# Performance work log

Measured on AMD Instinct MI355X. Metric: run time of the kernel, lower is better.

Reference implementation:

```python
import jax, jax.numpy as jnp
import numpy as np

D = 128
N = 262144

def setup_inputs() -> dict:
    key = jax.random.key(0)
    ks = jax.random.split(key, 10)
    inp = {
        'member_embeddings': 0.1 * jax.random.normal(ks[0], (N, D), dtype=jnp.float32),
        'item_embedding': 0.1 * jax.random.normal(ks[1], (D,), dtype=jnp.float32),
        # nn.Linear params (torch convention: y = x @ W.T + b)
        'W_c1': jax.random.normal(ks[2], (D, D), dtype=jnp.float32) / np.sqrt(D),
        'b_c1': jnp.zeros((D,), dtype=jnp.float32),
        'W_c2': jax.random.normal(ks[3], (D, D), dtype=jnp.float32) / np.sqrt(D),
        'b_c2': jnp.zeros((D,), dtype=jnp.float32),
        'w_pa': jax.random.normal(ks[4], (D,), dtype=jnp.float32) / np.sqrt(D),  # peer_attention weight (1,D) squeezed
        'b_pa': jnp.zeros((), dtype=jnp.float32),
        'w_vc': jax.random.normal(ks[5], (D,), dtype=jnp.float32) / np.sqrt(D),  # v_c weight (1,D) squeezed
        'b_vc': jnp.zeros((), dtype=jnp.float32),
    }
    return inp

def reference(member_embeddings, item_embedding, W_c1, b_c1, W_c2, b_c2, w_pa, b_pa, w_vc, b_vc):
    E = member_embeddings  # [N, D]
    # SP: self persistence scores  alpha_SP_i = u_i^T v
    sp = E @ item_embedding  # [N]
    # Peer scores are per-member scalars shared across all exclusion sets.
    s = E @ w_pa + b_pa                       # [N]
    m = jnp.max(s)
    e = jnp.exp(s - m)                        # [N]
    S = jnp.sum(e)                            # scalar
    eE = e[:, None] * E                       # [N, D]
    sum_eE = jnp.sum(eE, axis=0)              # [D]
    # softmax over peers excluding i (exact: softmax is shift-invariant)
    denom = S - e                             # [N]
    peer_agg = (sum_eE[None, :] - eE) / denom[:, None]  # [N, D]
    # PI: v_c^T ReLU(W_c1 u_i + W_c2 peer_agg_i + b)
    h = E @ W_c1.T + b_c1 + peer_agg @ W_c2.T + b_c2     # [N, D]
    pi = jax.nn.relu(h) @ w_vc + b_vc                    # [N]  (dropout = identity in eval)
    alpha = jnp.float32(1.0)
    beta = jnp.float32(1.0)
    attention_weights = jax.nn.softmax(alpha * sp + beta * pi, axis=0)  # [N]
    group_embedding = attention_weights @ E               # [D]
    return (group_embedding, attention_weights)
```

## Files before the change

### kernel.cpp

```cpp
#include <hip/hip_runtime.h>

#define DIM 128

typedef __attribute__((ext_vector_type(8))) short bf16x8;
typedef __attribute__((ext_vector_type(4))) float f32x4;

#define WS_B12    0
#define WS_C      128
#define WS_SUMEE  256
#define WS_S      384
#define WS_ZB     416
#define WS_GEB    512
#define WS_WBF    4608
#define WS_EEP    20992
#define WS_SEP    152064
#define WS_SP     153088
#define WS_E      415232
#define WS_WEXP   677376

__device__ __forceinline__ unsigned short f2bf(float f) {
    union { float f; unsigned u; } v; v.f = f;
    unsigned r = v.u + 0x7fffu + ((v.u >> 16) & 1u);
    return (unsigned short)(r >> 16);
}

__device__ __forceinline__ float bfbits(unsigned u) {
    union { unsigned u; float f; } v; v.u = u;
    return v.f;
}

__global__ __launch_bounds__(256) void k1_init(const float* __restrict__ Wc1,
                                               const float* __restrict__ Wc2,
                                               const float* __restrict__ bc1,
                                               const float* __restrict__ bc2,
                                               float* __restrict__ ws) {
    int gid = blockIdx.x * 256 + threadIdx.x;
    unsigned short* wbf = (unsigned short*)(ws + WS_WBF);
    if (gid < 32768) {
        int n = gid >> 7, k = gid & 127;
        float v = (n < 128) ? Wc1[n * 128 + k] : Wc2[(n - 128) * 128 + k];
        wbf[gid] = f2bf(v);
    }
    if (gid < 4096) ws[WS_GEB + gid] = 0.f;
    if (gid < 128) ws[WS_B12 + gid] = bc1[gid] + bc2[gid];
    if (gid < 64) ws[WS_ZB + gid] = 0.f;
}

__global__ __launch_bounds__(256) void k2_stats(const float* __restrict__ E,
                                                const float* __restrict__ v,
                                                const float* __restrict__ wpa,
                                                const float* __restrict__ bpa,
                                                float* __restrict__ ws) {
    __shared__ float red[16][128];
    __shared__ float redS[16];
    int t = threadIdx.x;
    int wave = t >> 6, lane = t & 63;
    int cl = lane & 15, rs = lane >> 4;
    int row0 = blockIdx.x * 256;
    const float4* E4 = (const float4*)E;

    float4 va = ((const float4*)v)[cl];
    float4 vb = ((const float4*)v)[16 + cl];
    float4 pa = ((const float4*)wpa)[cl];
    float4 pb = ((const float4*)wpa)[16 + cl];
    float bias = bpa[0];

    float4 acc0 = {0.f, 0.f, 0.f, 0.f}, acc1 = {0.f, 0.f, 0.f, 0.f};
    float se = 0.f;
    float* sp_ws = ws + WS_SP;
    float* e_ws = ws + WS_E;

#pragma unroll 4
    for (int it = 0; it < 16; ++it) {
        int row = row0 + it * 16 + wave * 4 + rs;
        float4 x0 = E4[row * 32 + cl];
        float4 x1 = E4[row * 32 + 16 + cl];
        float dv = x0.x * va.x + x0.y * va.y + x0.z * va.z + x0.w * va.w
                 + x1.x * vb.x + x1.y * vb.y + x1.z * vb.z + x1.w * vb.w;
        float dp = x0.x * pa.x + x0.y * pa.y + x0.z * pa.z + x0.w * pa.w
                 + x1.x * pb.x + x1.y * pb.y + x1.z * pb.z + x1.w * pb.w;
        for (int off = 1; off < 16; off <<= 1) {
            dv += __shfl_xor(dv, off);
            dp += __shfl_xor(dp, off);
        }
        float e = __expf(dp + bias);
        if (cl == 0) {
            sp_ws[row] = dv;
            e_ws[row] = e;
            se += e;
        }
        acc0.x += e * x0.x; acc0.y += e * x0.y; acc0.z += e * x0.z; acc0.w += e * x0.w;
        acc1.x += e * x1.x; acc1.y += e * x1.y; acc1.z += e * x1.z; acc1.w += e * x1.w;
    }
    int rr = wave * 4 + rs;
    float* dst = red[rr];
    dst[cl * 4 + 0] = acc0.x; dst[cl * 4 + 1] = acc0.y;
    dst[cl * 4 + 2] = acc0.z; dst[cl * 4 + 3] = acc0.w;
    dst[64 + cl * 4 + 0] = acc1.x; dst[64 + cl * 4 + 1] = acc1.y;
    dst[64 + cl * 4 + 2] = acc1.z; dst[64 + cl * 4 + 3] = acc1.w;
    if (cl == 0) redS[rr] = se;
    __syncthreads();
    if (t < 128) {
        float s = 0.f;
#pragma unroll
        for (int r = 0; r < 16; ++r) s += red[r][t];
        ws[WS_EEP + t * 1024 + blockIdx.x] = s;
    }
    if (t == 0) {
        float s = 0.f;
#pragma unroll
        for (int r = 0; r < 16; ++r) s += redS[r];
        ws[WS_SEP + blockIdx.x] = s;
    }
}

__global__ __launch_bounds__(256) void k2b_reduce(float* __restrict__ ws) {
    __shared__ float r4[4];
    int t = threadIdx.x, blk = blockIdx.x;
    const float* src = (blk < 128) ? (ws + WS_EEP + blk * 1024) : (ws + WS_SEP);
    float s = src[t] + src[t + 256] + src[t + 512] + src[t + 768];
    for (int off = 1; off < 64; off <<= 1) s += __shfl_xor(s, off);
    if ((t & 63) == 0) r4[t >> 6] = s;
    __syncthreads();
    if (t == 0) {
        float tot = r4[0] + r4[1] + r4[2] + r4[3];
        if (blk < 128) ws[WS_SUMEE + blk] = tot;
        else ws[WS_S] = tot;
    }
}

__global__ __launch_bounds__(128) void k3_c(const float* __restrict__ Wc2,
                                            float* __restrict__ ws) {
    int j = threadIdx.x;
    const float4* row = (const float4*)(Wc2 + j * 128);
    const float4* se = (const float4*)(ws + WS_SUMEE);
    float4 s4 = {0.f, 0.f, 0.f, 0.f};
#pragma unroll
    for (int k = 0; k < 32; ++k) {
        float4 a = row[k], b = se[k];
        s4.x += a.x * b.x; s4.y += a.y * b.y; s4.z += a.z * b.z; s4.w += a.w * b.w;
    }
    ws[WS_C + j] = s4.x + s4.y + s4.z + s4.w;
}

__global__ __launch_bounds__(512, 6) void k4_main(const float* __restrict__ E,
                                                  const float* __restrict__ wvc,
                                                  const float* __restrict__ bvc_p,
                                                  float* __restrict__ ws) {
    __shared__ unsigned short Elds[64 * 136];
    __shared__ float pim[8][64];
    __shared__ float gep[8][128];
    __shared__ float e_lds[64], dinv_lds[64];
    __shared__ float zw[8];

    int t = threadIdx.x;
    int w = t >> 6, lane = t & 63, cl = lane & 15, q = lane >> 4;
    int row0 = blockIdx.x * 64;
    const unsigned short* wbf = (const unsigned short*)(ws + WS_WBF);

    int j = w * 16 + cl;
    float cj = ws[WS_C + j];
    float b12j = ws[WS_B12 + j];
    float wvcj = wvc[j];
    float bvc = bvc_p[0];
    int r0 = w * 8 + q * 2;
    float sp0 = ws[WS_SP + row0 + r0];
    float sp1 = ws[WS_SP + row0 + r0 + 1];

    bf16x8 bfr[2][4];
#pragma unroll
    for (int c2 = 0; c2 < 2; ++c2) {
        int ct = w + c2 * 8;
#pragma unroll
        for (int kt = 0; kt < 4; ++kt)
            bfr[c2][kt] = *(const bf16x8*)(wbf + (ct * 16 + cl) * 128 + kt * 32 + q * 8);
    }

    const float4* E4 = (const float4*)E + (size_t)row0 * 32;
#pragma unroll
    for (int i = 0; i < 4; ++i) {
        int idx = t + 512 * i;
        int row = idx >> 5, kq = idx & 31;
        float4 x = E4[idx];
        unsigned p0 = (unsigned)f2bf(x.x) | ((unsigned)f2bf(x.y) << 16);
        unsigned p1 = (unsigned)f2bf(x.z) | ((unsigned)f2bf(x.w) << 16);
        *(uint2*)&Elds[row * 136 + kq * 4] = make_uint2(p0, p1);
    }
    if (t < 64) {
        float Sv = ws[WS_S];
        float ev = ws[WS_E + row0 + t];
        e_lds[t] = ev;
        dinv_lds[t] = 1.0f / (Sv - ev);
    }
    __syncthreads();

    f32x4 acc[4][2];
#pragma unroll
    for (int rt = 0; rt < 4; ++rt) {
        acc[rt][0] = (f32x4){0.f, 0.f, 0.f, 0.f};
        acc[rt][1] = (f32x4){0.f, 0.f, 0.f, 0.f};
    }
#pragma unroll
    for (int rt = 0; rt < 4; ++rt) {
        bf16x8 a[4];
#pragma unroll
        for (int kt = 0; kt < 4; ++kt)
            a[kt] = *(const bf16x8*)&Elds[(rt * 16 + cl) * 136 + kt * 32 + q * 8];
#pragma unroll
        for (int kt = 0; kt < 4; ++kt) {
            acc[rt][0] = __builtin_amdgcn_mfma_f32_16x16x32_bf16(a[kt], bfr[0][kt], acc[rt][0], 0, 0, 0);
            acc[rt][1] = __builtin_amdgcn_mfma_f32_16x16x32_bf16(a[kt], bfr[1][kt], acc[rt][1], 0, 0, 0);
        }
    }

#pragma unroll
    for (int rt = 0; rt < 4; ++rt) {
#pragma unroll
        for (int reg = 0; reg < 4; ++reg) {
            int row_it = rt * 16 + q * 4 + reg;
            float er = e_lds[row_it];
            float dinv = dinv_lds[row_it];
            float h = acc[rt][0][reg] + b12j + (cj - er * acc[rt][1][reg]) * dinv;
            float p = wvcj * fmaxf(h, 0.f);
            p += __shfl_xor(p, 1);
            p += __shfl_xor(p, 2);
            p += __shfl_xor(p, 4);
            p += __shfl_xor(p, 8);
            if (cl == 0) pim[w][row_it] = p;
        }
    }
    __syncthreads();

    float pi0 = 0.f, pi1 = 0.f;
#pragma unroll
    for (int wv = 0; wv < 8; ++wv) {
        pi0 += pim[wv][r0];
        pi1 += pim[wv][r0 + 1];
    }
    float we0 = __expf(sp0 + bvc + pi0);
    float we1 = __expf(sp1 + bvc + pi1);
    if (cl == 0) {
        ws[WS_WEXP + row0 + r0] = we0;
        ws[WS_WEXP + row0 + r0 + 1] = we1;
    }
    float z = we0 + we1;
    z += __shfl_xor(z, 16);
    z += __shfl_xor(z, 32);
    if (lane == 0) zw[w] = z;

    float acc8[8] = {0.f, 0.f, 0.f, 0.f, 0.f, 0.f, 0.f, 0.f};
#pragma unroll
    for (int rr = 0; rr < 2; ++rr) {
        int r = r0 + rr;
        float wer = rr ? we1 : we0;
        uint4 u = *(const uint4*)&Elds[r * 136 + cl * 8];
        acc8[0] += wer * bfbits(u.x << 16);
        acc8[1] += wer * bfbits(u.x & 0xffff0000u);
        acc8[2] += wer * bfbits(u.y << 16);
        acc8[3] += wer * bfbits(u.y & 0xffff0000u);
        acc8[4] += wer * bfbits(u.z << 16);
        acc8[5] += wer * bfbits(u.z & 0xffff0000u);
        acc8[6] += wer * bfbits(u.w << 16);
        acc8[7] += wer * bfbits(u.w & 0xffff0000u);
    }
#pragma unroll
    for (int jj = 0; jj < 8; ++jj) {
        acc8[jj] += __shfl_xor(acc8[jj], 16);
        acc8[jj] += __shfl_xor(acc8[jj], 32);
    }
    if (lane < 16) {
        *(float4*)&gep[w][cl * 8] = (float4){acc8[0], acc8[1], acc8[2], acc8[3]};
        *(float4*)&gep[w][cl * 8 + 4] = (float4){acc8[4], acc8[5], acc8[6], acc8[7]};
    }
    __syncthreads();

    if (t < 128) {
        float tot = 0.f;
#pragma unroll
        for (int wv = 0; wv < 8; ++wv) tot += gep[wv][t];
        atomicAdd(&ws[WS_GEB + (blockIdx.x & 31) * 128 + t], tot);
    }
    if (t == 128) {
        float zs = zw[0] + zw[1] + zw[2] + zw[3] + zw[4] + zw[5] + zw[6] + zw[7];
        atomicAdd(&ws[WS_ZB + (blockIdx.x & 63)], zs);
    }
}

__global__ __launch_bounds__(256) void k5_final(const float* __restrict__ ws,
                                                float* __restrict__ out) {
    int t = threadIdx.x, blk = blockIdx.x;
    float z = ws[WS_ZB + (t & 63)];
    for (int off = 1; off < 64; off <<= 1) z += __shfl_xor(z, off);
    float invZ = 1.0f / z;
    if (blk < 1024) {
        int i = blk * 256 + t;
        out[128 + i] = ws[WS_WEXP + i] * invZ;
    } else if (t < 128) {
        float s = 0.f;
#pragma unroll
        for (int b = 0; b < 32; ++b) s += ws[WS_GEB + b * 128 + t];
        out[t] = s * invZ;
    }
}

extern "C" void kernel_launch(void* const* d_in, const int* in_sizes, int n_in,
                              void* d_out, int out_size, void* d_ws, size_t ws_size,
                              hipStream_t stream) {
    const float* E   = (const float*)d_in[0];
    const float* v   = (const float*)d_in[1];
    const float* Wc1 = (const float*)d_in[2];
    const float* bc1 = (const float*)d_in[3];
    const float* Wc2 = (const float*)d_in[4];
    const float* bc2 = (const float*)d_in[5];
    const float* wpa = (const float*)d_in[6];
    const float* bpa = (const float*)d_in[7];
    const float* wvc = (const float*)d_in[8];
    const float* bvc = (const float*)d_in[9];
    float* ws  = (float*)d_ws;
    float* out = (float*)d_out;

    k1_init<<<128, 256, 0, stream>>>(Wc1, Wc2, bc1, bc2, ws);
    k2_stats<<<1024, 256, 0, stream>>>(E, v, wpa, bpa, ws);
    k2b_reduce<<<129, 256, 0, stream>>>(ws);
    k3_c<<<1, 128, 0, stream>>>(Wc2, ws);
    k4_main<<<4096, 512, 0, stream>>>(E, wvc, bvc, ws);
    k5_final<<<1025, 256, 0, stream>>>(ws, out);
}
```

Measured before the change: 274.8 us.

## Write bf16 copy of E in stats pass and read it directly in main kernel

The stats kernel now also writes a bf16 copy of the member embeddings to workspace, and the main kernel reads MFMA A-operands and the weighted-sum rows from that copy in global memory instead of re-reading fp32 E and staging it through LDS. This halves the main kernel's read traffic and removes its LDS staging and one barrier. In exchange it adds a 64 MB write in the stats pass, and its operand loads become uncoalesced, strided global loads that are likely to be served from L2. The launch-bounds occupancy hint drops from 6 to 4, and the workspace must be large enough for the new buffer.

```diff
diff --git a/kernel.cpp b/kernel.cpp
--- a/kernel.cpp
+++ b/kernel.cpp
@@ -17,6 +17,7 @@
 #define WS_SP     153088
 #define WS_E      415232
 #define WS_WEXP   677376
+#define WS_EBF    939520
 
 __device__ __forceinline__ unsigned short f2bf(float f) {
     union { float f; unsigned u; } v; v.f = f;
@@ -58,6 +59,7 @@
     int cl = lane & 15, rs = lane >> 4;
     int row0 = blockIdx.x * 256;
     const float4* E4 = (const float4*)E;
+    unsigned short* ebf = (unsigned short*)(ws + WS_EBF);
 
     float4 va = ((const float4*)v)[cl];
     float4 vb = ((const float4*)v)[16 + cl];
@@ -75,6 +77,14 @@
         int row = row0 + it * 16 + wave * 4 + rs;
         float4 x0 = E4[row * 32 + cl];
         float4 x1 = E4[row * 32 + 16 + cl];
+        unsigned p0 = (unsigned)f2bf(x0.x) | ((unsigned)f2bf(x0.y) << 16);
+        unsigned p1 = (unsigned)f2bf(x0.z) | ((unsigned)f2bf(x0.w) << 16);
+        unsigned p2 = (unsigned)f2bf(x1.x) | ((unsigned)f2bf(x1.y) << 16);
+        unsigned p3 = (unsigned)f2bf(x1.z) | ((unsigned)f2bf(x1.w) << 16);
+        unsigned short* er = ebf + (size_t)row * 128;
+        *(uint2*)(er + cl * 4) = make_uint2(p0, p1);
+        *(uint2*)(er + 64 + cl * 4) = make_uint2(p2, p3);
+
         float dv = x0.x * va.x + x0.y * va.y + x0.z * va.z + x0.w * va.w
                  + x1.x * vb.x + x1.y * vb.y + x1.z * vb.z + x1.w * vb.w;
         float dp = x0.x * pa.x + x0.y * pa.y + x0.z * pa.z + x0.w * pa.w
@@ -143,11 +153,9 @@
     ws[WS_C + j] = s4.x + s4.y + s4.z + s4.w;
 }
 
-__global__ __launch_bounds__(512, 6) void k4_main(const float* __restrict__ E,
-                                                  const float* __restrict__ wvc,
+__global__ __launch_bounds__(512, 4) void k4_main(const float* __restrict__ wvc,
                                                   const float* __restrict__ bvc_p,
                                                   float* __restrict__ ws) {
-    __shared__ unsigned short Elds[64 * 136];
     __shared__ float pim[8][64];
     __shared__ float gep[8][128];
     __shared__ float e_lds[64], dinv_lds[64];
@@ -157,6 +165,7 @@
     int w = t >> 6, lane = t & 63, cl = lane & 15, q = lane >> 4;
     int row0 = blockIdx.x * 64;
     const unsigned short* wbf = (const unsigned short*)(ws + WS_WBF);
+    const unsigned short* ebf = (const unsigned short*)(ws + WS_EBF);
 
     int j = w * 16 + cl;
     float cj = ws[WS_C + j];
@@ -176,23 +185,12 @@
             bfr[c2][kt] = *(const bf16x8*)(wbf + (ct * 16 + cl) * 128 + kt * 32 + q * 8);
     }
 
-    const float4* E4 = (const float4*)E + (size_t)row0 * 32;
-#pragma unroll
-    for (int i = 0; i < 4; ++i) {
-        int idx = t + 512 * i;
-        int row = idx >> 5, kq = idx & 31;
-        float4 x = E4[idx];
-        unsigned p0 = (unsigned)f2bf(x.x) | ((unsigned)f2bf(x.y) << 16);
-        unsigned p1 = (unsigned)f2bf(x.z) | ((unsigned)f2bf(x.w) << 16);
-        *(uint2*)&Elds[row * 136 + kq * 4] = make_uint2(p0, p1);
-    }
     if (t < 64) {
         float Sv = ws[WS_S];
         float ev = ws[WS_E + row0 + t];
         e_lds[t] = ev;
         dinv_lds[t] = 1.0f / (Sv - ev);
     }
-    __syncthreads();
 
     f32x4 acc[4][2];
 #pragma unroll
@@ -202,16 +200,18 @@
     }
 #pragma unroll
     for (int rt = 0; rt < 4; ++rt) {
+        const unsigned short* arow = ebf + (size_t)(row0 + rt * 16 + cl) * 128 + q * 8;
         bf16x8 a[4];
 #pragma unroll
         for (int kt = 0; kt < 4; ++kt)
-            a[kt] = *(const bf16x8*)&Elds[(rt * 16 + cl) * 136 + kt * 32 + q * 8];
+            a[kt] = *(const bf16x8*)(arow + kt * 32);
 #pragma unroll
         for (int kt = 0; kt < 4; ++kt) {
             acc[rt][0] = __builtin_amdgcn_mfma_f32_16x16x32_bf16(a[kt], bfr[0][kt], acc[rt][0], 0, 0, 0);
             acc[rt][1] = __builtin_amdgcn_mfma_f32_16x16x32_bf16(a[kt], bfr[1][kt], acc[rt][1], 0, 0, 0);
         }
     }
+    __syncthreads();
 
 #pragma unroll
     for (int rt = 0; rt < 4; ++rt) {
@@ -251,9 +251,8 @@
     float acc8[8] = {0.f, 0.f, 0.f, 0.f, 0.f, 0.f, 0.f, 0.f};
 #pragma unroll
     for (int rr = 0; rr < 2; ++rr) {
-        int r = r0 + rr;
         float wer = rr ? we1 : we0;
-        uint4 u = *(const uint4*)&Elds[r * 136 + cl * 8];
+        uint4 u = *(const uint4*)(ebf + (size_t)(row0 + r0 + rr) * 128 + cl * 8);
         acc8[0] += wer * bfbits(u.x << 16);
         acc8[1] += wer * bfbits(u.x & 0xffff0000u);
         acc8[2] += wer * bfbits(u.y << 16);
@@ -323,6 +322,6 @@
     k2_stats<<<1024, 256, 0, stream>>>(E, v, wpa, bpa, ws);
     k2b_reduce<<<129, 256, 0, stream>>>(ws);
     k3_c<<<1, 128, 0, stream>>>(Wc2, ws);
-    k4_main<<<4096, 512, 0, stream>>>(E, wvc, bvc, ws);
+    k4_main<<<4096, 512, 0, stream>>>(wvc, bvc, ws);
     k5_final<<<1025, 256, 0, stream>>>(ws, out);
 }
```

After: 327.2 us. 1.19x slower.

## Restructure main kernel into smaller blocks with swizzled LDS and tree reduction

Applied to the files above, without the earlier changes.

The main kernel now runs 256-thread blocks over 32 rows each. Each wave keeps its A fragments in registers and loops over two column groups, loading the W fragments per pass instead of holding all B fragments resident. The LDS tile drops its padding and uses an XOR swizzle to avoid bank conflicts. The group-embedding atomics are replaced by per-block partial writes plus a separate reduction kernel, and the stats kernel uses twice as many blocks. These changes aim to raise occupancy and remove atomic contention, at the cost of an extra launch, more workspace traffic and repeated weight loads from cache.

```diff
diff --git a/kernel.cpp b/kernel.cpp
--- a/kernel.cpp
+++ b/kernel.cpp
@@ -1,27 +1,26 @@
 #include <hip/hip_runtime.h>
-
-#define DIM 128
 
 typedef __attribute__((ext_vector_type(8))) short bf16x8;
 typedef __attribute__((ext_vector_type(4))) float f32x4;
 
 #define WS_B12    0
-#define WS_C      128
-#define WS_SUMEE  256
-#define WS_S      384
-#define WS_ZB     416
-#define WS_GEB    512
-#define WS_WBF    4608
-#define WS_EEP    20992
-#define WS_SEP    152064
-#define WS_SP     153088
-#define WS_E      415232
-#define WS_WEXP   677376
-
-__device__ __forceinline__ unsigned short f2bf(float f) {
+#define WS_CPK    128
+#define WS_SUMEE  640
+#define WS_S      768
+#define WS_ZB     800
+#define WS_WBF    896
+#define WS_EEP    17280
+#define WS_SEP    279424
+#define WS_SP     281472
+#define WS_E      543616
+#define WS_WEXP   805760
+#define WS_GOUT   1067904
+#define WS_G2     2116480
+
+__device__ __forceinline__ unsigned f2bf(float f) {
     union { float f; unsigned u; } v; v.f = f;
     unsigned r = v.u + 0x7fffu + ((v.u >> 16) & 1u);
-    return (unsigned short)(r >> 16);
+    return r >> 16;
 }
 
 __device__ __forceinline__ float bfbits(unsigned u) {
@@ -39,9 +38,8 @@
     if (gid < 32768) {
         int n = gid >> 7, k = gid & 127;
         float v = (n < 128) ? Wc1[n * 128 + k] : Wc2[(n - 128) * 128 + k];
-        wbf[gid] = f2bf(v);
-    }
-    if (gid < 4096) ws[WS_GEB + gid] = 0.f;
+        wbf[gid] = (unsigned short)f2bf(v);
+    }
     if (gid < 128) ws[WS_B12 + gid] = bc1[gid] + bc2[gid];
     if (gid < 64) ws[WS_ZB + gid] = 0.f;
 }
@@ -56,7 +54,7 @@
     int t = threadIdx.x;
     int wave = t >> 6, lane = t & 63;
     int cl = lane & 15, rs = lane >> 4;
-    int row0 = blockIdx.x * 256;
+    int row0 = blockIdx.x * 128;
     const float4* E4 = (const float4*)E;
 
     float4 va = ((const float4*)v)[cl];
@@ -71,7 +69,7 @@
     float* e_ws = ws + WS_E;
 
 #pragma unroll 4
-    for (int it = 0; it < 16; ++it) {
+    for (int it = 0; it < 8; ++it) {
         int row = row0 + it * 16 + wave * 4 + rs;
         float4 x0 = E4[row * 32 + cl];
         float4 x1 = E4[row * 32 + 16 + cl];
@@ -104,7 +102,7 @@
         float s = 0.f;
 #pragma unroll
         for (int r = 0; r < 16; ++r) s += red[r][t];
-        ws[WS_EEP + t * 1024 + blockIdx.x] = s;
+        ws[WS_EEP + t * 2048 + blockIdx.x] = s;
     }
     if (t == 0) {
         float s = 0.f;
@@ -117,8 +115,10 @@
 __global__ __launch_bounds__(256) void k2b_reduce(float* __restrict__ ws) {
     __shared__ float r4[4];
     int t = threadIdx.x, blk = blockIdx.x;
-    const float* src = (blk < 128) ? (ws + WS_EEP + blk * 1024) : (ws + WS_SEP);
-    float s = src[t] + src[t + 256] + src[t + 512] + src[t + 768];
+    const float* src = (blk < 128) ? (ws + WS_EEP + blk * 2048) : (ws + WS_SEP);
+    float s = 0.f;
+#pragma unroll
+    for (int k = 0; k < 8; ++k) s += src[t + 256 * k];
     for (int off = 1; off < 64; off <<= 1) s += __shfl_xor(s, off);
     if ((t & 63) == 0) r4[t >> 6] = s;
     __syncthreads();
@@ -130,6 +130,7 @@
 }
 
 __global__ __launch_bounds__(128) void k3_c(const float* __restrict__ Wc2,
+                                            const float* __restrict__ wvc,
                                             float* __restrict__ ws) {
     int j = threadIdx.x;
     const float4* row = (const float4*)(Wc2 + j * 128);
@@ -140,109 +141,107 @@
         float4 a = row[k], b = se[k];
         s4.x += a.x * b.x; s4.y += a.y * b.y; s4.z += a.z * b.z; s4.w += a.w * b.w;
     }
-    ws[WS_C + j] = s4.x + s4.y + s4.z + s4.w;
-}
-
-__global__ __launch_bounds__(512, 6) void k4_main(const float* __restrict__ E,
-                                                  const float* __restrict__ wvc,
+    float cj = s4.x + s4.y + s4.z + s4.w;
+    *(float4*)(ws + WS_CPK + j * 4) = (float4){cj, ws[WS_B12 + j], wvc[j], 0.f};
+}
+
+__global__ __launch_bounds__(256, 4) void k4_main(const float* __restrict__ E,
                                                   const float* __restrict__ bvc_p,
                                                   float* __restrict__ ws) {
-    __shared__ unsigned short Elds[64 * 136];
-    __shared__ float pim[8][64];
-    __shared__ float gep[8][128];
-    __shared__ float e_lds[64], dinv_lds[64];
-    __shared__ float zw[8];
+    __shared__ unsigned short Elds[32 * 128];
+    __shared__ float pim[4][32];
+    __shared__ float gep[4][128];
+    __shared__ float zw[4];
 
     int t = threadIdx.x;
     int w = t >> 6, lane = t & 63, cl = lane & 15, q = lane >> 4;
-    int row0 = blockIdx.x * 64;
+    int row0 = blockIdx.x * 32;
     const unsigned short* wbf = (const unsigned short*)(ws + WS_WBF);
 
-    int j = w * 16 + cl;
-    float cj = ws[WS_C + j];
-    float b12j = ws[WS_B12 + j];
-    float wvcj = wvc[j];
+    const float4* E4 = (const float4*)E + (size_t)row0 * 32;
+#pragma unroll
+    for (int i = 0; i < 4; ++i) {
+        int idx = t + 256 * i;
+        int row = idx >> 5, kq = idx & 31;
+        float4 x = E4[idx];
+        unsigned p0 = f2bf(x.x) | (f2bf(x.y) << 16);
+        unsigned p1 = f2bf(x.z) | (f2bf(x.w) << 16);
+        int cc = (kq >> 1) ^ ((row & 1) << 2);
+        *(uint2*)&Elds[row * 128 + cc * 8 + (kq & 1) * 4] = make_uint2(p0, p1);
+    }
+
+    float Sv = ws[WS_S];
     float bvc = bvc_p[0];
+    float4 eA = *(const float4*)(ws + WS_E + row0 + q * 4);
+    float4 eB = *(const float4*)(ws + WS_E + row0 + 16 + q * 4);
+    float dinvA[4], dinvB[4];
+#pragma unroll
+    for (int r = 0; r < 4; ++r) {
+        dinvA[r] = 1.0f / (Sv - ((const float*)&eA)[r]);
+        dinvB[r] = 1.0f / (Sv - ((const float*)&eB)[r]);
+    }
     int r0 = w * 8 + q * 2;
     float sp0 = ws[WS_SP + row0 + r0];
     float sp1 = ws[WS_SP + row0 + r0 + 1];
-
-    bf16x8 bfr[2][4];
-#pragma unroll
-    for (int c2 = 0; c2 < 2; ++c2) {
-        int ct = w + c2 * 8;
+    __syncthreads();
+
+    bf16x8 a[2][4];
+#pragma unroll
+    for (int rt = 0; rt < 2; ++rt) {
+        int row = rt * 16 + cl;
+        int sw = (row & 1) << 2;
+        const unsigned short* rbase = Elds + row * 128;
 #pragma unroll
         for (int kt = 0; kt < 4; ++kt)
-            bfr[c2][kt] = *(const bf16x8*)(wbf + (ct * 16 + cl) * 128 + kt * 32 + q * 8);
-    }
-
-    const float4* E4 = (const float4*)E + (size_t)row0 * 32;
-#pragma unroll
-    for (int i = 0; i < 4; ++i) {
-        int idx = t + 512 * i;
-        int row = idx >> 5, kq = idx & 31;
-        float4 x = E4[idx];
-        unsigned p0 = (unsigned)f2bf(x.x) | ((unsigned)f2bf(x.y) << 16);
-        unsigned p1 = (unsigned)f2bf(x.z) | ((unsigned)f2bf(x.w) << 16);
-        *(uint2*)&Elds[row * 136 + kq * 4] = make_uint2(p0, p1);
-    }
-    if (t < 64) {
-        float Sv = ws[WS_S];
-        float ev = ws[WS_E + row0 + t];
-        e_lds[t] = ev;
-        dinv_lds[t] = 1.0f / (Sv - ev);
-    }
-    __syncthreads();
-
-    f32x4 acc[4][2];
-#pragma unroll
-    for (int rt = 0; rt < 4; ++rt) {
-        acc[rt][0] = (f32x4){0.f, 0.f, 0.f, 0.f};
-        acc[rt][1] = (f32x4){0.f, 0.f, 0.f, 0.f};
-    }
-#pragma unroll
-    for (int rt = 0; rt < 4; ++rt) {
-        bf16x8 a[4];
-#pragma unroll
-        for (int kt = 0; kt < 4; ++kt)
-            a[kt] = *(const bf16x8*)&Elds[(rt * 16 + cl) * 136 + kt * 32 + q * 8];
+            a[rt][kt] = *(const bf16x8*)(rbase + ((((kt << 2) + q) ^ sw) << 3));
+    }
+
+    float pirow[2][4] = {{0.f, 0.f, 0.f, 0.f}, {0.f, 0.f, 0.f, 0.f}};
+#pragma unroll 1
+    for (int pp = 0; pp < 2; ++pp) {
+        int j = (w + pp * 4) * 16 + cl;
+        float4 cc = *(const float4*)(ws + WS_CPK + j * 4);
+        bf16x8 b0[4], b1[4];
 #pragma unroll
         for (int kt = 0; kt < 4; ++kt) {
-            acc[rt][0] = __builtin_amdgcn_mfma_f32_16x16x32_bf16(a[kt], bfr[0][kt], acc[rt][0], 0, 0, 0);
-            acc[rt][1] = __builtin_amdgcn_mfma_f32_16x16x32_bf16(a[kt], bfr[1][kt], acc[rt][1], 0, 0, 0);
-        }
-    }
-
-#pragma unroll
-    for (int rt = 0; rt < 4; ++rt) {
+            b0[kt] = *(const bf16x8*)(wbf + (size_t)j * 128 + kt * 32 + q * 8);
+            b1[kt] = *(const bf16x8*)(wbf + (size_t)(128 + j) * 128 + kt * 32 + q * 8);
+        }
+#pragma unroll
+        for (int rt = 0; rt < 2; ++rt) {
+            f32x4 acc0 = {0.f, 0.f, 0.f, 0.f}, acc1 = {0.f, 0.f, 0.f, 0.f};
+#pragma unroll
+            for (int kt = 0; kt < 4; ++kt) {
+                acc0 = __builtin_amdgcn_mfma_f32_16x16x32_bf16(a[rt][kt], b0[kt], acc0, 0, 0, 0);
+                acc1 = __builtin_amdgcn_mfma_f32_16x16x32_bf16(a[rt][kt], b1[kt], acc1, 0, 0, 0);
+            }
+            const float* ee = rt ? (const float*)&eB : (const float*)&eA;
+            const float* dd = rt ? dinvB : dinvA;
+#pragma unroll
+            for (int reg = 0; reg < 4; ++reg) {
+                float h = acc0[reg] + cc.y + (cc.x - ee[reg] * acc1[reg]) * dd[reg];
+                pirow[rt][reg] += cc.z * fmaxf(h, 0.f);
+            }
+        }
+    }
+#pragma unroll
+    for (int rt = 0; rt < 2; ++rt)
 #pragma unroll
         for (int reg = 0; reg < 4; ++reg) {
-            int row_it = rt * 16 + q * 4 + reg;
-            float er = e_lds[row_it];
-            float dinv = dinv_lds[row_it];
-            float h = acc[rt][0][reg] + b12j + (cj - er * acc[rt][1][reg]) * dinv;
-            float p = wvcj * fmaxf(h, 0.f);
+            float p = pirow[rt][reg];
             p += __shfl_xor(p, 1);
             p += __shfl_xor(p, 2);
             p += __shfl_xor(p, 4);
             p += __shfl_xor(p, 8);
-            if (cl == 0) pim[w][row_it] = p;
-        }
-    }
-    __syncthreads();
-
-    float pi0 = 0.f, pi1 = 0.f;
-#pragma unroll
-    for (int wv = 0; wv < 8; ++wv) {
-        pi0 += pim[wv][r0];
-        pi1 += pim[wv][r0 + 1];
-    }
+            if (cl == 0) pim[w][rt * 16 + q * 4 + reg] = p;
+        }
+    __syncthreads();
+
+    float pi0 = pim[0][r0] + pim[1][r0] + pim[2][r0] + pim[3][r0];
+    float pi1 = pim[0][r0 + 1] + pim[1][r0 + 1] + pim[2][r0 + 1] + pim[3][r0 + 1];
     float we0 = __expf(sp0 + bvc + pi0);
     float we1 = __expf(sp1 + bvc + pi1);
-    if (cl == 0) {
-        ws[WS_WEXP + row0 + r0] = we0;
-        ws[WS_WEXP + row0 + r0 + 1] = we1;
-    }
+    if (cl == 0) *(float2*)(ws + WS_WEXP + row0 + r0) = make_float2(we0, we1);
     float z = we0 + we1;
     z += __shfl_xor(z, 16);
     z += __shfl_xor(z, 32);
@@ -253,7 +252,8 @@
     for (int rr = 0; rr < 2; ++rr) {
         int r = r0 + rr;
         float wer = rr ? we1 : we0;
-        uint4 u = *(const uint4*)&Elds[r * 136 + cl * 8];
+        int cc = cl ^ (rr << 2);
+        uint4 u = *(const uint4*)(Elds + r * 128 + cc * 8);
         acc8[0] += wer * bfbits(u.x << 16);
         acc8[1] += wer * bfbits(u.x & 0xffff0000u);
         acc8[2] += wer * bfbits(u.y << 16);
@@ -275,15 +275,20 @@
     __syncthreads();
 
     if (t < 128) {
-        float tot = 0.f;
-#pragma unroll
-        for (int wv = 0; wv < 8; ++wv) tot += gep[wv][t];
-        atomicAdd(&ws[WS_GEB + (blockIdx.x & 31) * 128 + t], tot);
-    }
-    if (t == 128) {
-        float zs = zw[0] + zw[1] + zw[2] + zw[3] + zw[4] + zw[5] + zw[6] + zw[7];
-        atomicAdd(&ws[WS_ZB + (blockIdx.x & 63)], zs);
-    }
+        float tot = gep[0][t] + gep[1][t] + gep[2][t] + gep[3][t];
+        ws[WS_GOUT + (size_t)blockIdx.x * 128 + t] = tot;
+    }
+    if (t == 0)
+        atomicAdd(&ws[WS_ZB + (blockIdx.x & 63)], zw[0] + zw[1] + zw[2] + zw[3]);
+}
+
+__global__ __launch_bounds__(128) void k4b_ge(float* __restrict__ ws) {
+    int t = threadIdx.x, b = blockIdx.x;
+    const float* src = ws + WS_GOUT + (size_t)b * 32 * 128;
+    float s = 0.f;
+#pragma unroll 8
+    for (int k = 0; k < 32; ++k) s += src[k * 128 + t];
+    ws[WS_G2 + b * 128 + t] = s;
 }
 
 __global__ __launch_bounds__(256) void k5_final(const float* __restrict__ ws,
@@ -297,8 +302,8 @@
         out[128 + i] = ws[WS_WEXP + i] * invZ;
     } else if (t < 128) {
         float s = 0.f;
-#pragma unroll
-        for (int b = 0; b < 32; ++b) s += ws[WS_GEB + b * 128 + t];
+#pragma unroll 8
+        for (int k = 0; k < 256; ++k) s += ws[WS_G2 + k * 128 + t];
         out[t] = s * invZ;
     }
 }
@@ -320,9 +325,10 @@
     float* out = (float*)d_out;
 
     k1_init<<<128, 256, 0, stream>>>(Wc1, Wc2, bc1, bc2, ws);
-    k2_stats<<<1024, 256, 0, stream>>>(E, v, wpa, bpa, ws);
+    k2_stats<<<2048, 256, 0, stream>>>(E, v, wpa, bpa, ws);
     k2b_reduce<<<129, 256, 0, stream>>>(ws);
-    k3_c<<<1, 128, 0, stream>>>(Wc2, ws);
-    k4_main<<<4096, 512, 0, stream>>>(E, wvc, bvc, ws);
+    k3_c<<<1, 128, 0, stream>>>(Wc2, wvc, ws);
+    k4_main<<<8192, 256, 0, stream>>>(E, bvc, ws);
+    k4b_ge<<<256, 128, 0, stream>>>(ws);
     k5_final<<<1025, 256, 0, stream>>>(ws, out);
 }
```

Result: slower. 310.3 us (+12.9%).
